# Kernel optimization log

Hardware: AMD Instinct MI355X
Metric: run time of the kernel (lower is better)

## Reference

```python
import jax, jax.numpy as jnp
import numpy as np

DIM, NH, HD = 1536, 12, 128
C = HD // 2            # 64 complex (half) dims per head
BANDS = (C - 2 * (C // 3), C // 3, C // 3)   # (22, 21, 21) for T/H/W
EPS = 1e-6
F, Hg, Wg = 6, 20, 32
S = F * Hg * Wg
MAX_LEN = 1024


def _rope_tables(max_len=MAX_LEN):
    # Wan-style 1D rope params per band, concatenated along channel dim -> [max_len, 64]
    pos = np.arange(max_len, dtype=np.float64)
    cos_l, sin_l = [], []
    for bd in BANDS:
        inv = 1.0 / (10000.0 ** (np.arange(bd, dtype=np.float64) / bd))
        ang = np.outer(pos, inv)
        cos_l.append(np.cos(ang))
        sin_l.append(np.sin(ang))
    return (np.concatenate(cos_l, 1).astype(np.float32),
            np.concatenate(sin_l, 1).astype(np.float32))


def setup_inputs() -> dict:
    key = jax.random.key(0)
    ks = jax.random.split(key, 8)
    std = 0.02
    fc, fs = _rope_tables()
    return {
        "x": jax.random.normal(ks[0], (1, S, DIM), jnp.float32),
        "Wq": jax.random.normal(ks[1], (DIM, DIM), jnp.float32) * std,
        "bq": jnp.zeros((DIM,), jnp.float32),
        "Wk": jax.random.normal(ks[2], (DIM, DIM), jnp.float32) * std,
        "bk": jnp.zeros((DIM,), jnp.float32),
        "Wv": jax.random.normal(ks[3], (DIM, DIM), jnp.float32) * std,
        "bv": jnp.zeros((DIM,), jnp.float32),
        "Wo": jax.random.normal(ks[4], (DIM, DIM), jnp.float32) * std,
        "bo": jnp.zeros((DIM,), jnp.float32),
        "gq": jnp.ones((DIM,), jnp.float32),
        "gk": jnp.ones((DIM,), jnp.float32),
        "freqs_cos": jnp.asarray(fc),
        "freqs_sin": jnp.asarray(fs),
        "f": F, "h": Hg, "w": Wg,
    }


def _rmsnorm(t, g):
    t = t.astype(jnp.float32)
    return t * jax.lax.rsqrt(jnp.mean(t * t, axis=-1, keepdims=True) + EPS) * g


def _grid_freqs(tab, f, h, w):
    # tab: [max_len, 64] -> [f*h*w, 64] via T/H/W band broadcast (mirrors torch expand+cat)
    o1, o2 = BANDS[0], BANDS[0] + BANDS[1]
    t = jnp.broadcast_to(tab[:f, None, None, :o1], (f, h, w, BANDS[0]))
    hh = jnp.broadcast_to(tab[None, :h, None, o1:o2], (f, h, w, BANDS[1]))
    ww = jnp.broadcast_to(tab[None, None, :w, o2:C], (f, h, w, BANDS[2]))
    return jnp.concatenate([t, hh, ww], axis=-1).reshape(f * h * w, 1, C)


def _rope_apply(t, fc, fs):
    # t: [B, S, n, d]; complex mul (a+ib)*(cos+isin) on pairs of channels
    B, Sl, n, d = t.shape
    tr = t.astype(jnp.float32).reshape(B, Sl, n, C, 2)
    a, b = tr[..., 0], tr[..., 1]
    fc = fc[None]  # [1, S, 1, C]
    fs = fs[None]
    out_r = a * fc - b * fs
    out_i = a * fs + b * fc
    return jnp.stack([out_r, out_i], axis=-1).reshape(B, Sl, n, d)


def reference(x, Wq, bq, Wk, bk, Wv, bv, Wo, bo, gq, gk, freqs_cos, freqs_sin, f, h, w):
    B, Sl, _ = x.shape
    q = _rmsnorm(x @ Wq.T + bq, gq).reshape(B, Sl, NH, HD)
    k = _rmsnorm(x @ Wk.T + bk, gk).reshape(B, Sl, NH, HD)
    v = (x @ Wv.T + bv).reshape(B, Sl, NH, HD)

    fc = _grid_freqs(freqs_cos, f, h, w)
    fs = _grid_freqs(freqs_sin, f, h, w)
    q = _rope_apply(q, fc, fs)
    k = _rope_apply(k, fc, fs)

    scale = 1.0 / jnp.sqrt(jnp.float32(HD))
    scores = jnp.einsum('bqnd,bknd->bnqk', q, k) * scale
    p = jax.nn.softmax(scores, axis=-1)
    o = jnp.einsum('bnqk,bknd->bqnd', p, v.astype(jnp.float32))
    o = o.reshape(B, Sl, DIM)
    return o @ Wo.T + bo
```

## Files before the change

### kernel.cpp

```cpp
#include <hip/hip_runtime.h>
#include <hip/hip_bf16.h>
#include <cstdint>

#define DIM 1536
#define NHEADS 12
#define HD 128
#define SEQ 3840

typedef float f32x4 __attribute__((ext_vector_type(4)));
typedef __bf16 bf16x8 __attribute__((ext_vector_type(8)));
typedef __bf16 bf16x4 __attribute__((ext_vector_type(4)));
typedef __bf16 bf16x2 __attribute__((ext_vector_type(2)));
typedef unsigned int u32;
typedef u32 u32x4 __attribute__((ext_vector_type(4)));

#define GLLD(g, l) __builtin_amdgcn_global_load_lds( \
    (const __attribute__((address_space(1))) void*)(g), \
    (__attribute__((address_space(3))) void*)(l), 16, 0, 0)

__global__ __launch_bounds__(256) void cvt_bf16_5(
    const float* __restrict__ s0, const float* __restrict__ s1, const float* __restrict__ s2,
    const float* __restrict__ s3, const float* __restrict__ s4,
    __bf16* __restrict__ d0, __bf16* __restrict__ d1, __bf16* __restrict__ d2,
    __bf16* __restrict__ d3, __bf16* __restrict__ d4,
    int n4_0, int n4_w) {
    const float* src; __bf16* dst; int n4;
    switch (blockIdx.y) {
        case 0: src = s0; dst = d0; n4 = n4_0; break;
        case 1: src = s1; dst = d1; n4 = n4_w; break;
        case 2: src = s2; dst = d2; n4 = n4_w; break;
        case 3: src = s3; dst = d3; n4 = n4_w; break;
        default: src = s4; dst = d4; n4 = n4_w; break;
    }
    int i = blockIdx.x * 256 + threadIdx.x;
    if (i < n4) {
        f32x4 v = ((const f32x4*)src)[i];
        bf16x4 o;
        o[0] = (__bf16)v[0]; o[1] = (__bf16)v[1];
        o[2] = (__bf16)v[2]; o[3] = (__bf16)v[3];
        ((bf16x4*)dst)[i] = o;
    }
}

template <int OUTF32>
__global__ __launch_bounds__(256) void gemm_bt(
    const __bf16* __restrict__ A,
    const __bf16* __restrict__ B0, const __bf16* __restrict__ B1, const __bf16* __restrict__ B2,
    const float* __restrict__ bias0, const float* __restrict__ bias1, const float* __restrict__ bias2,
    void* __restrict__ C0v, void* __restrict__ C1v, void* __restrict__ C2v,
    int N, int K) {
    const __bf16* B = B0; const float* bias = bias0; void* Cv = C0v;
    if (blockIdx.z == 1) { B = B1; bias = bias1; Cv = C1v; }
    else if (blockIdx.z == 2) { B = B2; bias = bias2; Cv = C2v; }

    __shared__ __bf16 As[2][128 * 32];
    __shared__ __bf16 Bs[2][128 * 32];

    const int t = threadIdx.x;
    const int w = t >> 6;
    const int lane = t & 63;
    const int lr = lane & 15, lg = lane >> 4;
    const int wr = (w >> 1) * 64, wc = (w & 1) * 64;
    const int wb = w * 512;

    const long long rowA = (long long)blockIdx.y * 128 + (t >> 2);
    const long long rowB = (long long)blockIdx.x * 128 + (t >> 2);
    const int kcol = (t & 3) * 8;

    const __bf16* pa0 = A + rowA * K + kcol;
    const __bf16* pa1 = pa0 + 64LL * K;
    const __bf16* pb0 = B + rowB * K + kcol;
    const __bf16* pb1 = pb0 + 64LL * K;

    f32x4 acc[4][4] = {};

    auto stage = [&](int kk, int b) {
        GLLD(pa0 + kk, &As[b][wb]);
        GLLD(pa1 + kk, &As[b][2048 + wb]);
        GLLD(pb0 + kk, &Bs[b][wb]);
        GLLD(pb1 + kk, &Bs[b][2048 + wb]);
    };

    stage(0, 0);
    int buf = 0;
#pragma unroll 1
    for (int kk = 0; kk < K; kk += 32) {
        __syncthreads();
        if (kk + 32 < K) stage(kk + 32, buf ^ 1);
        bf16x8 af[4], bfr[4];
#pragma unroll
        for (int m = 0; m < 4; m++)
            af[m] = *(const bf16x8*)(&As[buf][(wr + m * 16 + lr) * 32 + lg * 8]);
#pragma unroll
        for (int n = 0; n < 4; n++)
            bfr[n] = *(const bf16x8*)(&Bs[buf][(wc + n * 16 + lr) * 32 + lg * 8]);
#pragma unroll
        for (int m = 0; m < 4; m++)
#pragma unroll
            for (int n = 0; n < 4; n++)
                acc[m][n] = __builtin_amdgcn_mfma_f32_16x16x32_bf16(af[m], bfr[n], acc[m][n], 0, 0, 0);
        buf ^= 1;
    }

    const int cb = blockIdx.x * 128 + wc;
    const int rb_ = blockIdx.y * 128 + wr;
#pragma unroll
    for (int n = 0; n < 4; n++) {
        int col = cb + n * 16 + lr;
        float bv = bias[col];
#pragma unroll
        for (int m = 0; m < 4; m++) {
            int row0 = rb_ + m * 16 + lg * 4;
#pragma unroll
            for (int r = 0; r < 4; r++) {
                float v = acc[m][n][r] + bv;
                if (OUTF32) ((float*)Cv)[(long long)(row0 + r) * N + col] = v;
                else ((__bf16*)Cv)[(long long)(row0 + r) * N + col] = (__bf16)v;
            }
        }
    }
}

__global__ __launch_bounds__(256) void norm_rope(
    const __bf16* __restrict__ pre,
    const float* __restrict__ gvec,
    const float* __restrict__ fcos,
    const float* __restrict__ fsin,
    __bf16* __restrict__ out) {
    const int s = blockIdx.x;
    const int t = threadIdx.x;
    float a[3], b[3];
    float ss = 0.f;
#pragma unroll
    for (int j = 0; j < 3; j++) {
        int p = t + 256 * j;
        bf16x2 v = *(const bf16x2*)(pre + (size_t)s * DIM + 2 * p);
        a[j] = (float)v[0]; b[j] = (float)v[1];
        ss += a[j] * a[j] + b[j] * b[j];
    }
    for (int off = 32; off; off >>= 1) ss += __shfl_down(ss, off);
    __shared__ float red[4];
    if ((t & 63) == 0) red[t >> 6] = ss;
    __syncthreads();
    float mean = (red[0] + red[1] + red[2] + red[3]) * (1.f / DIM);
    float rms = rsqrtf(mean + 1e-6f);
    const int fi = s / 640, hi2 = (s % 640) >> 5, wi = s & 31;
#pragma unroll
    for (int j = 0; j < 3; j++) {
        int p = t + 256 * j;
        int c = p & 63;
        int pos = (c < 22) ? fi : ((c < 43) ? hi2 : wi);
        float fc = fcos[pos * 64 + c];
        float fs = fsin[pos * 64 + c];
        float av = a[j] * rms * gvec[2 * p];
        float bv = b[j] * rms * gvec[2 * p + 1];
        float orr = av * fc - bv * fs;
        float oi = av * fs + bv * fc;
        int hh = p >> 6;
        bf16x2 o; o[0] = (__bf16)orr; o[1] = (__bf16)oi;
        *(bf16x2*)(out + ((size_t)hh * SEQ + s) * HD + 2 * c) = o;
    }
}

__global__ __launch_bounds__(256) void transpose_bf16(
    const __bf16* __restrict__ in, __bf16* __restrict__ out) {
    __shared__ __bf16 tile[64][68];
    const int t = threadIdx.x;
    const int sb = blockIdx.x * 64, cb = blockIdx.y * 64;
    const int tx = t & 15, ty = t >> 4;
#pragma unroll
    for (int i = 0; i < 4; i++) {
        int r = ty + i * 16;
        bf16x4 v = *(const bf16x4*)(in + (size_t)(sb + r) * DIM + cb + tx * 4);
        *(bf16x4*)&tile[r][tx * 4] = v;
    }
    __syncthreads();
    int s0 = sb + tx * 4;
    int j = (s0 >> 2) & 7;
    int u = (j < 4) ? (j << 1) : ((j << 1) - 7);
    int sp = (s0 & ~31) + (u << 2);
#pragma unroll
    for (int i = 0; i < 4; i++) {
        int c = ty + i * 16;
        bf16x4 v;
        v[0] = tile[tx * 4 + 0][c]; v[1] = tile[tx * 4 + 1][c];
        v[2] = tile[tx * 4 + 2][c]; v[3] = tile[tx * 4 + 3][c];
        *(bf16x4*)(out + (size_t)(cb + c) * SEQ + sp) = v;
    }
}

__global__ __launch_bounds__(384, 1) void attn(
    const __bf16* __restrict__ Q,
    const __bf16* __restrict__ Kk,
    const __bf16* __restrict__ Vp,
    __bf16* __restrict__ O) {
    __shared__ __bf16 Ks[2][64 * 128];
    __shared__ __bf16 Vs[2][128 * 64];

    const int bid = blockIdx.x;
    const int task = (bid & 7) * 30 + (bid >> 3);
    const int h = task / 20;
    const int qb = task % 20;
    const int t = threadIdx.x;
    const int wv = t >> 6;
    const int lane = t & 63;
    const int lq = lane & 15, g = lane >> 4;
    const int q0 = qb * 192 + wv * 32;

    const __bf16* Qh = Q + (size_t)h * SEQ * HD;
    const __bf16* Kh = Kk + (size_t)h * SEQ * HD;
    const __bf16* Vh = Vp + (size_t)h * HD * SEQ;

    bf16x8 qf[2][4];
#pragma unroll
    for (int qg = 0; qg < 2; qg++)
#pragma unroll
        for (int c = 0; c < 4; c++)
            qf[qg][c] = *(const bf16x8*)(Qh + (size_t)(q0 + qg * 16 + lq) * HD + c * 32 + g * 8);

    f32x4 acc[8][2] = {};
    float m[2] = {-1e30f, -1e30f}, l[2] = {0.f, 0.f};
    const float SCL2 = 0.1275365308119098f;
    const float THR_RAW = 90.50966799187809f;

    const int krow_in = lane >> 4;
    const int vrow_in = lane >> 3;
    const int vce = (((lane & 7) ^ (lane >> 3))) * 8;
    auto stage = [&](int kv0, int b) {
        for (int c = wv; c < 32; c += 6) {
            if (c < 16) {
                int r = c * 4 + krow_in;
                int cb = ((lane & 15) * 16) ^ ((r & 7) << 4);
                GLLD(Kh + (size_t)(kv0 + r) * HD + (cb >> 1), &Ks[b][c * 512]);
            } else {
                int cc = c - 16;
                int rd = cc * 8 + vrow_in;
                GLLD(Vh + (size_t)rd * SEQ + kv0 + vce, &Vs[b][cc * 512]);
            }
        }
    };

    stage(0, 0);
    int buf = 0;
    const int kswz = (lq & 7) << 3;
#pragma unroll 1
    for (int i = 0; i < 60; i++) {
        __syncthreads();
        if (i + 1 < 60) stage((i + 1) * 64, buf ^ 1);
        const __bf16* Kb_ = &Ks[buf][0];
        const __bf16* Vb_ = &Vs[buf][0];

#pragma unroll
        for (int s = 0; s < 2; s++) {
            f32x4 sc[2][2] = {};
            __builtin_amdgcn_s_setprio(1);
#pragma unroll
            for (int c = 0; c < 4; c++) {
                int cb = (c * 32 + g * 8) ^ kswz;
                bf16x8 k0 = *(const bf16x8*)(Kb_ + (s * 32 + lq) * 128 + cb);
                bf16x8 k1 = *(const bf16x8*)(Kb_ + (s * 32 + 16 + lq) * 128 + cb);
                sc[0][0] = __builtin_amdgcn_mfma_f32_16x16x32_bf16(k0, qf[0][c], sc[0][0], 0, 0, 0);
                sc[0][1] = __builtin_amdgcn_mfma_f32_16x16x32_bf16(k0, qf[1][c], sc[0][1], 0, 0, 0);
                sc[1][0] = __builtin_amdgcn_mfma_f32_16x16x32_bf16(k1, qf[0][c], sc[1][0], 0, 0, 0);
                sc[1][1] = __builtin_amdgcn_mfma_f32_16x16x32_bf16(k1, qf[1][c], sc[1][1], 0, 0, 0);
            }
            __builtin_amdgcn_s_setprio(0);

            bf16x8 pa[2];
#pragma unroll
            for (int qg = 0; qg < 2; qg++) {
                float pm = fmaxf(fmaxf(fmaxf(sc[0][qg][0], sc[0][qg][1]), fmaxf(sc[0][qg][2], sc[0][qg][3])),
                                 fmaxf(fmaxf(sc[1][qg][0], sc[1][qg][1]), fmaxf(sc[1][qg][2], sc[1][qg][3])));
                pm = fmaxf(pm, __shfl_xor(pm, 16));
                pm = fmaxf(pm, __shfl_xor(pm, 32));
                if (!__all(pm <= m[qg] + THR_RAW)) {
                    float mn = fmaxf(m[qg], pm);
                    float al = __builtin_amdgcn_exp2f(SCL2 * (m[qg] - mn));
                    m[qg] = mn;
                    l[qg] *= al;
#pragma unroll
                    for (int dt = 0; dt < 8; dt++)
#pragma unroll
                        for (int r = 0; r < 4; r++) acc[dt][qg][r] *= al;
                }
                float ms = SCL2 * m[qg];
                float p[8], ls = 0.f;
#pragma unroll
                for (int r = 0; r < 4; r++) { p[r] = __builtin_amdgcn_exp2f(SCL2 * sc[0][qg][r] - ms); ls += p[r]; }
#pragma unroll
                for (int r = 0; r < 4; r++) { p[4 + r] = __builtin_amdgcn_exp2f(SCL2 * sc[1][qg][r] - ms); ls += p[4 + r]; }
                ls += __shfl_xor(ls, 16);
                ls += __shfl_xor(ls, 32);
                l[qg] += ls;
#pragma unroll
                for (int i2 = 0; i2 < 8; i2++) pa[qg][i2] = (__bf16)p[i2];
            }

            bf16x8 vf[8];
#pragma unroll
            for (int dt = 0; dt < 8; dt++)
                vf[dt] = *(const bf16x8*)(Vb_ + (dt * 16 + lq) * 64 + ((s * 32 + g * 8) ^ kswz));
            __builtin_amdgcn_s_setprio(1);
#pragma unroll
            for (int dt = 0; dt < 8; dt++) {
                acc[dt][0] = __builtin_amdgcn_mfma_f32_16x16x32_bf16(vf[dt], pa[0], acc[dt][0], 0, 0, 0);
                acc[dt][1] = __builtin_amdgcn_mfma_f32_16x16x32_bf16(vf[dt], pa[1], acc[dt][1], 0, 0, 0);
            }
            __builtin_amdgcn_s_setprio(0);
        }
        buf ^= 1;
    }

#pragma unroll
    for (int qg = 0; qg < 2; qg++) {
        float inv = 1.f / l[qg];
#pragma unroll
        for (int dt = 0; dt < 8; dt++) {
            bf16x4 o;
#pragma unroll
            for (int r = 0; r < 4; r++) o[r] = (__bf16)(acc[dt][qg][r] * inv);
            *(bf16x4*)(O + (size_t)(q0 + qg * 16 + lq) * DIM + h * HD + dt * 16 + g * 4) = o;
        }
    }
}

extern "C" void kernel_launch(void* const* d_in, const int* in_sizes, int n_in,
                              void* d_out, int out_size, void* d_ws, size_t ws_size,
                              hipStream_t stream) {
    const float* x = (const float*)d_in[0];
    const float* Wq = (const float*)d_in[1];
    const float* bq = (const float*)d_in[2];
    const float* Wk = (const float*)d_in[3];
    const float* bk = (const float*)d_in[4];
    const float* Wv = (const float*)d_in[5];
    const float* bv = (const float*)d_in[6];
    const float* Wo = (const float*)d_in[7];
    const float* bo = (const float*)d_in[8];
    const float* gq = (const float*)d_in[9];
    const float* gk = (const float*)d_in[10];
    const float* fcos = (const float*)d_in[11];
    const float* fsin = (const float*)d_in[12];
    float* out = (float*)d_out;

    char* ws = (char*)d_ws;
    const size_t SZ_SD = (size_t)SEQ * DIM * 2;
    const size_t SZ_W = (size_t)DIM * DIM * 2;
    __bf16* xb   = (__bf16*)ws;            ws += SZ_SD;
    __bf16* Wqb  = (__bf16*)ws;            ws += SZ_W;
    __bf16* Wkb  = (__bf16*)ws;            ws += SZ_W;
    __bf16* Wvb  = (__bf16*)ws;            ws += SZ_W;
    __bf16* Wob  = (__bf16*)ws;            ws += SZ_W;
    __bf16* qpre = (__bf16*)ws;            ws += SZ_SD;
    __bf16* kpre = (__bf16*)ws;            ws += SZ_SD;
    __bf16* vpre = (__bf16*)ws;            ws += SZ_SD;
    __bf16* Kb   = (__bf16*)ws;            ws += SZ_SD;
    __bf16* Vtb  = (__bf16*)ws;            ws += SZ_SD;
    __bf16* Qb = xb;
    __bf16* ob = qpre;

    const int n4_x = SEQ * DIM / 4;
    const int n4_w = DIM * DIM / 4;
    cvt_bf16_5<<<dim3((n4_x + 255) / 256, 5), 256, 0, stream>>>(
        x, Wq, Wk, Wv, Wo, xb, Wqb, Wkb, Wvb, Wob, n4_x, n4_w);

    gemm_bt<0><<<dim3(DIM / 128, SEQ / 128, 3), 256, 0, stream>>>(
        xb, Wqb, Wkb, Wvb, bq, bk, bv, qpre, kpre, vpre, DIM, DIM);

    norm_rope<<<SEQ, 256, 0, stream>>>(qpre, gq, fcos, fsin, Qb);
    norm_rope<<<SEQ, 256, 0, stream>>>(kpre, gk, fcos, fsin, Kb);
    transpose_bf16<<<dim3(SEQ / 64, DIM / 64), 256, 0, stream>>>(vpre, Vtb);

    attn<<<dim3(240), 384, 0, stream>>>(Qb, Kb, Vtb, ob);

    gemm_bt<1><<<dim3(DIM / 128, SEQ / 128, 1), 256, 0, stream>>>(
        ob, Wob, Wob, Wob, bo, bo, bo, out, out, out, DIM, DIM);
}
```

Measured before the change: 320.8 us.

## Enlarge GEMM tiles with triple-buffered pipeline, fuse norm launches, defer softmax reductions

The projection GEMMs move to a 256x128 tile with three LDS stages, explicit vmcnt waits and split barriers, so loads overlap compute and each block reuses more data. The Q and K norm/rope kernels are merged into a single launch. In attention, the row-max shuffle now runs only when the rescale branch fires, and the row-sum cross-lane reduction is postponed to the epilogue. V fragment loads are also hoisted ahead of the softmax. These changes cut barriers, shuffles and launches, but the larger tiles give fewer blocks and raise register pressure.

Result: faster. 287.1 us (-10.5%).

```diff
diff --git a/kernel.cpp b/kernel.cpp
--- a/kernel.cpp
+++ b/kernel.cpp
@@ -6,6 +6,8 @@
 #define NHEADS 12
 #define HD 128
 #define SEQ 3840
+#define SCL2F 0.1275365308119098f
+#define THRRAW 90.50966799187809f
 
 typedef float f32x4 __attribute__((ext_vector_type(4)));
 typedef __bf16 bf16x8 __attribute__((ext_vector_type(8)));
@@ -43,7 +45,7 @@
 }
 
 template <int OUTF32>
-__global__ __launch_bounds__(256) void gemm_bt(
+__global__ __launch_bounds__(256, 2) void gemm256(
     const __bf16* __restrict__ A,
     const __bf16* __restrict__ B0, const __bf16* __restrict__ B1, const __bf16* __restrict__ B2,
     const float* __restrict__ bias0, const float* __restrict__ bias1, const float* __restrict__ bias2,
@@ -53,67 +55,86 @@
     if (blockIdx.z == 1) { B = B1; bias = bias1; Cv = C1v; }
     else if (blockIdx.z == 2) { B = B2; bias = bias2; Cv = C2v; }
 
-    __shared__ __bf16 As[2][128 * 32];
-    __shared__ __bf16 Bs[2][128 * 32];
+    __shared__ __bf16 sA[3][256 * 32];
+    __shared__ __bf16 sB[3][128 * 32];
 
     const int t = threadIdx.x;
-    const int w = t >> 6;
-    const int lane = t & 63;
+    const int wid = t >> 6, lane = t & 63;
     const int lr = lane & 15, lg = lane >> 4;
-    const int wr = (w >> 1) * 64, wc = (w & 1) * 64;
-    const int wb = w * 512;
-
-    const long long rowA = (long long)blockIdx.y * 128 + (t >> 2);
-    const long long rowB = (long long)blockIdx.x * 128 + (t >> 2);
-    const int kcol = (t & 3) * 8;
-
-    const __bf16* pa0 = A + rowA * K + kcol;
-    const __bf16* pa1 = pa0 + 64LL * K;
-    const __bf16* pb0 = B + rowB * K + kcol;
-    const __bf16* pb1 = pb0 + 64LL * K;
-
-    f32x4 acc[4][4] = {};
-
-    auto stage = [&](int kk, int b) {
-        GLLD(pa0 + kk, &As[b][wb]);
-        GLLD(pa1 + kk, &As[b][2048 + wb]);
-        GLLD(pb0 + kk, &Bs[b][wb]);
-        GLLD(pb1 + kk, &Bs[b][2048 + wb]);
+    const int wr = (wid >> 1) * 128, wc = (wid & 1) * 64;
+
+    const __bf16* pa = A + ((long long)blockIdx.y * 256 + (t >> 2)) * K + (t & 3) * 8;
+    const __bf16* pb = B + ((long long)blockIdx.x * 128 + (t >> 2)) * K + (t & 3) * 8;
+    const int ldsbase = wid * 512;
+
+    auto stage = [&](int kk, int bufi) {
+#pragma unroll
+        for (int r = 0; r < 4; r++)
+            GLLD(pa + (long long)(r * 64) * K + kk, &sA[bufi][r * 2048 + ldsbase]);
+#pragma unroll
+        for (int r = 0; r < 2; r++)
+            GLLD(pb + (long long)(r * 64) * K + kk, &sB[bufi][r * 2048 + ldsbase]);
     };
 
+    f32x4 acc[8][4] = {};
+    const int NT = K / 32;
+
     stage(0, 0);
-    int buf = 0;
+    stage(32, 1);
+    asm volatile("s_waitcnt vmcnt(6)" ::: "memory");
+    __builtin_amdgcn_s_barrier();
+    __builtin_amdgcn_sched_barrier(0);
+
+    int c0 = 0, c2 = 2;
 #pragma unroll 1
-    for (int kk = 0; kk < K; kk += 32) {
-        __syncthreads();
-        if (kk + 32 < K) stage(kk + 32, buf ^ 1);
-        bf16x8 af[4], bfr[4];
-#pragma unroll
-        for (int m = 0; m < 4; m++)
-            af[m] = *(const bf16x8*)(&As[buf][(wr + m * 16 + lr) * 32 + lg * 8]);
-#pragma unroll
-        for (int n = 0; n < 4; n++)
-            bfr[n] = *(const bf16x8*)(&Bs[buf][(wc + n * 16 + lr) * 32 + lg * 8]);
-#pragma unroll
-        for (int m = 0; m < 4; m++)
-#pragma unroll
-            for (int n = 0; n < 4; n++)
-                acc[m][n] = __builtin_amdgcn_mfma_f32_16x16x32_bf16(af[m], bfr[n], acc[m][n], 0, 0, 0);
-        buf ^= 1;
+    for (int i = 0; i < NT; i++) {
+        const __bf16* sAc = &sA[0][0] + c0 * (256 * 32);
+        const __bf16* sBc = &sB[0][0] + c0 * (128 * 32);
+        bf16x8 af[8], bfr[4];
+#pragma unroll
+        for (int mI = 0; mI < 8; mI++)
+            af[mI] = *(const bf16x8*)(sAc + (wr + mI * 16 + lr) * 32 + lg * 8);
+#pragma unroll
+        for (int nI = 0; nI < 4; nI++)
+            bfr[nI] = *(const bf16x8*)(sBc + (wc + nI * 16 + lr) * 32 + lg * 8);
+        if (i + 2 < NT) stage((i + 2) * 32, c2);
+
+        __builtin_amdgcn_s_setprio(1);
+#pragma unroll
+        for (int mI = 0; mI < 8; mI++) {
+            acc[mI][0] = __builtin_amdgcn_mfma_f32_16x16x32_bf16(af[mI], bfr[0], acc[mI][0], 0, 0, 0);
+            acc[mI][1] = __builtin_amdgcn_mfma_f32_16x16x32_bf16(af[mI], bfr[1], acc[mI][1], 0, 0, 0);
+        }
+        __builtin_amdgcn_s_setprio(0);
+        __builtin_amdgcn_s_barrier();
+        __builtin_amdgcn_s_setprio(1);
+#pragma unroll
+        for (int mI = 0; mI < 8; mI++) {
+            acc[mI][2] = __builtin_amdgcn_mfma_f32_16x16x32_bf16(af[mI], bfr[2], acc[mI][2], 0, 0, 0);
+            acc[mI][3] = __builtin_amdgcn_mfma_f32_16x16x32_bf16(af[mI], bfr[3], acc[mI][3], 0, 0, 0);
+        }
+        __builtin_amdgcn_s_setprio(0);
+
+        if (i + 2 < NT) asm volatile("s_waitcnt vmcnt(6)" ::: "memory");
+        else            asm volatile("s_waitcnt vmcnt(0)" ::: "memory");
+        __builtin_amdgcn_s_barrier();
+        __builtin_amdgcn_sched_barrier(0);
+        c0 = (c0 == 2) ? 0 : c0 + 1;
+        c2 = (c2 == 2) ? 0 : c2 + 1;
     }
 
     const int cb = blockIdx.x * 128 + wc;
-    const int rb_ = blockIdx.y * 128 + wr;
-#pragma unroll
-    for (int n = 0; n < 4; n++) {
-        int col = cb + n * 16 + lr;
+    const int rb_ = blockIdx.y * 256 + wr;
+#pragma unroll
+    for (int nI = 0; nI < 4; nI++) {
+        int col = cb + nI * 16 + lr;
         float bv = bias[col];
 #pragma unroll
-        for (int m = 0; m < 4; m++) {
-            int row0 = rb_ + m * 16 + lg * 4;
+        for (int mI = 0; mI < 8; mI++) {
+            int row0 = rb_ + mI * 16 + lg * 4;
 #pragma unroll
             for (int r = 0; r < 4; r++) {
-                float v = acc[m][n][r] + bv;
+                float v = acc[mI][nI][r] + bv;
                 if (OUTF32) ((float*)Cv)[(long long)(row0 + r) * N + col] = v;
                 else ((__bf16*)Cv)[(long long)(row0 + r) * N + col] = (__bf16)v;
             }
@@ -121,12 +142,14 @@
     }
 }
 
-__global__ __launch_bounds__(256) void norm_rope(
-    const __bf16* __restrict__ pre,
-    const float* __restrict__ gvec,
-    const float* __restrict__ fcos,
-    const float* __restrict__ fsin,
-    __bf16* __restrict__ out) {
+__global__ __launch_bounds__(256) void norm_rope2(
+    const __bf16* __restrict__ qpre, const __bf16* __restrict__ kpre,
+    const float* __restrict__ gq, const float* __restrict__ gk,
+    const float* __restrict__ fcos, const float* __restrict__ fsin,
+    __bf16* __restrict__ Qb, __bf16* __restrict__ Kb) {
+    const __bf16* pre = blockIdx.y ? kpre : qpre;
+    const float* gvec = blockIdx.y ? gk : gq;
+    __bf16* out = blockIdx.y ? Kb : Qb;
     const int s = blockIdx.x;
     const int t = threadIdx.x;
     float a[3], b[3];
@@ -190,13 +213,10 @@
 }
 
 __global__ __launch_bounds__(384, 1) void attn(
-    const __bf16* __restrict__ Q,
-    const __bf16* __restrict__ Kk,
-    const __bf16* __restrict__ Vp,
-    __bf16* __restrict__ O) {
+    const __bf16* __restrict__ Q, const __bf16* __restrict__ Kk,
+    const __bf16* __restrict__ Vp, __bf16* __restrict__ O) {
     __shared__ __bf16 Ks[2][64 * 128];
     __shared__ __bf16 Vs[2][128 * 64];
-
     const int bid = blockIdx.x;
     const int task = (bid & 7) * 30 + (bid >> 3);
     const int h = task / 20;
@@ -206,23 +226,18 @@
     const int lane = t & 63;
     const int lq = lane & 15, g = lane >> 4;
     const int q0 = qb * 192 + wv * 32;
-
     const __bf16* Qh = Q + (size_t)h * SEQ * HD;
     const __bf16* Kh = Kk + (size_t)h * SEQ * HD;
     const __bf16* Vh = Vp + (size_t)h * HD * SEQ;
-
     bf16x8 qf[2][4];
 #pragma unroll
     for (int qg = 0; qg < 2; qg++)
 #pragma unroll
         for (int c = 0; c < 4; c++)
             qf[qg][c] = *(const bf16x8*)(Qh + (size_t)(q0 + qg * 16 + lq) * HD + c * 32 + g * 8);
-
     f32x4 acc[8][2] = {};
-    float m[2] = {-1e30f, -1e30f}, l[2] = {0.f, 0.f};
-    const float SCL2 = 0.1275365308119098f;
-    const float THR_RAW = 90.50966799187809f;
-
+    float m[2] = {-1e30f, -1e30f};
+    float lp[2] = {0.f, 0.f};
     const int krow_in = lane >> 4;
     const int vrow_in = lane >> 3;
     const int vce = (((lane & 7) ^ (lane >> 3))) * 8;
@@ -239,7 +254,6 @@
             }
         }
     };
-
     stage(0, 0);
     int buf = 0;
     const int kswz = (lq & 7) << 3;
@@ -249,7 +263,6 @@
         if (i + 1 < 60) stage((i + 1) * 64, buf ^ 1);
         const __bf16* Kb_ = &Ks[buf][0];
         const __bf16* Vb_ = &Vs[buf][0];
-
 #pragma unroll
         for (int s = 0; s < 2; s++) {
             f32x4 sc[2][2] = {};
@@ -266,40 +279,37 @@
             }
             __builtin_amdgcn_s_setprio(0);
 
+            bf16x8 vf[8];
+#pragma unroll
+            for (int dt = 0; dt < 8; dt++)
+                vf[dt] = *(const bf16x8*)(Vb_ + (dt * 16 + lq) * 64 + ((s * 32 + g * 8) ^ kswz));
+
             bf16x8 pa[2];
 #pragma unroll
             for (int qg = 0; qg < 2; qg++) {
                 float pm = fmaxf(fmaxf(fmaxf(sc[0][qg][0], sc[0][qg][1]), fmaxf(sc[0][qg][2], sc[0][qg][3])),
                                  fmaxf(fmaxf(sc[1][qg][0], sc[1][qg][1]), fmaxf(sc[1][qg][2], sc[1][qg][3])));
-                pm = fmaxf(pm, __shfl_xor(pm, 16));
-                pm = fmaxf(pm, __shfl_xor(pm, 32));
-                if (!__all(pm <= m[qg] + THR_RAW)) {
+                if (!__all(pm <= m[qg] + THRRAW)) {
+                    pm = fmaxf(pm, __shfl_xor(pm, 16));
+                    pm = fmaxf(pm, __shfl_xor(pm, 32));
                     float mn = fmaxf(m[qg], pm);
-                    float al = __builtin_amdgcn_exp2f(SCL2 * (m[qg] - mn));
-                    m[qg] = mn;
-                    l[qg] *= al;
+                    float al = __builtin_amdgcn_exp2f(SCL2F * (m[qg] - mn));
+                    m[qg] = mn; lp[qg] *= al;
 #pragma unroll
                     for (int dt = 0; dt < 8; dt++)
 #pragma unroll
                         for (int r = 0; r < 4; r++) acc[dt][qg][r] *= al;
                 }
-                float ms = SCL2 * m[qg];
+                float ms = SCL2F * m[qg];
                 float p[8], ls = 0.f;
 #pragma unroll
-                for (int r = 0; r < 4; r++) { p[r] = __builtin_amdgcn_exp2f(SCL2 * sc[0][qg][r] - ms); ls += p[r]; }
-#pragma unroll
-                for (int r = 0; r < 4; r++) { p[4 + r] = __builtin_amdgcn_exp2f(SCL2 * sc[1][qg][r] - ms); ls += p[4 + r]; }
-                ls += __shfl_xor(ls, 16);
-                ls += __shfl_xor(ls, 32);
-                l[qg] += ls;
+                for (int r = 0; r < 4; r++) { p[r] = __builtin_amdgcn_exp2f(SCL2F * sc[0][qg][r] - ms); ls += p[r]; }
+#pragma unroll
+                for (int r = 0; r < 4; r++) { p[4 + r] = __builtin_amdgcn_exp2f(SCL2F * sc[1][qg][r] - ms); ls += p[4 + r]; }
+                lp[qg] += ls;
 #pragma unroll
                 for (int i2 = 0; i2 < 8; i2++) pa[qg][i2] = (__bf16)p[i2];
             }
-
-            bf16x8 vf[8];
-#pragma unroll
-            for (int dt = 0; dt < 8; dt++)
-                vf[dt] = *(const bf16x8*)(Vb_ + (dt * 16 + lq) * 64 + ((s * 32 + g * 8) ^ kswz));
             __builtin_amdgcn_s_setprio(1);
 #pragma unroll
             for (int dt = 0; dt < 8; dt++) {
@@ -310,10 +320,12 @@
         }
         buf ^= 1;
     }
-
 #pragma unroll
     for (int qg = 0; qg < 2; qg++) {
-        float inv = 1.f / l[qg];
+        float lps = lp[qg];
+        lps += __shfl_xor(lps, 16);
+        lps += __shfl_xor(lps, 32);
+        float inv = 1.f / lps;
 #pragma unroll
         for (int dt = 0; dt < 8; dt++) {
             bf16x4 o;
@@ -342,19 +354,19 @@
     const float* fsin = (const float*)d_in[12];
     float* out = (float*)d_out;
 
-    char* ws = (char*)d_ws;
+    char* p = (char*)d_ws;
     const size_t SZ_SD = (size_t)SEQ * DIM * 2;
     const size_t SZ_W = (size_t)DIM * DIM * 2;
-    __bf16* xb   = (__bf16*)ws;            ws += SZ_SD;
-    __bf16* Wqb  = (__bf16*)ws;            ws += SZ_W;
-    __bf16* Wkb  = (__bf16*)ws;            ws += SZ_W;
-    __bf16* Wvb  = (__bf16*)ws;            ws += SZ_W;
-    __bf16* Wob  = (__bf16*)ws;            ws += SZ_W;
-    __bf16* qpre = (__bf16*)ws;            ws += SZ_SD;
-    __bf16* kpre = (__bf16*)ws;            ws += SZ_SD;
-    __bf16* vpre = (__bf16*)ws;            ws += SZ_SD;
-    __bf16* Kb   = (__bf16*)ws;            ws += SZ_SD;
-    __bf16* Vtb  = (__bf16*)ws;            ws += SZ_SD;
+    __bf16* xb   = (__bf16*)p;  p += SZ_SD;
+    __bf16* Wqb  = (__bf16*)p;  p += SZ_W;
+    __bf16* Wkb  = (__bf16*)p;  p += SZ_W;
+    __bf16* Wvb  = (__bf16*)p;  p += SZ_W;
+    __bf16* Wob  = (__bf16*)p;  p += SZ_W;
+    __bf16* qpre = (__bf16*)p;  p += SZ_SD;
+    __bf16* kpre = (__bf16*)p;  p += SZ_SD;
+    __bf16* vpre = (__bf16*)p;  p += SZ_SD;
+    __bf16* Kb   = (__bf16*)p;  p += SZ_SD;
+    __bf16* Vtb  = (__bf16*)p;  p += SZ_SD;
     __bf16* Qb = xb;
     __bf16* ob = qpre;
 
@@ -363,15 +375,14 @@
     cvt_bf16_5<<<dim3((n4_x + 255) / 256, 5), 256, 0, stream>>>(
         x, Wq, Wk, Wv, Wo, xb, Wqb, Wkb, Wvb, Wob, n4_x, n4_w);
 
-    gemm_bt<0><<<dim3(DIM / 128, SEQ / 128, 3), 256, 0, stream>>>(
+    gemm256<0><<<dim3(DIM / 128, SEQ / 256, 3), 256, 0, stream>>>(
         xb, Wqb, Wkb, Wvb, bq, bk, bv, qpre, kpre, vpre, DIM, DIM);
 
-    norm_rope<<<SEQ, 256, 0, stream>>>(qpre, gq, fcos, fsin, Qb);
-    norm_rope<<<SEQ, 256, 0, stream>>>(kpre, gk, fcos, fsin, Kb);
+    norm_rope2<<<dim3(SEQ, 2), 256, 0, stream>>>(qpre, kpre, gq, gk, fcos, fsin, Qb, Kb);
     transpose_bf16<<<dim3(SEQ / 64, DIM / 64), 256, 0, stream>>>(vpre, Vtb);
 
     attn<<<dim3(240), 384, 0, stream>>>(Qb, Kb, Vtb, ob);
 
-    gemm_bt<1><<<dim3(DIM / 128, SEQ / 128, 1), 256, 0, stream>>>(
+    gemm256<1><<<dim3(DIM / 128, SEQ / 256, 1), 256, 0, stream>>>(
         ob, Wob, Wob, Wob, bo, bo, bo, out, out, out, DIM, DIM);
 }
```
